# Optimization experiments

Measured on AMD Instinct MI355X. Metric: run time of the kernel, lower is better.

The kernel has to match this reference:

```python
import jax, jax.numpy as jnp
import numpy as np

H, S, D = 64, 64, 4096  # num_heads, head_size, hidden_size (D = H*S)
EPS = 1e-5


def setup_inputs() -> dict:
    key = jax.random.key(0)
    ks = jax.random.split(key, 20)
    n = lambda i, shape, s=1.0: s * jax.random.normal(ks[i], shape, dtype=jnp.float32)
    u = lambda i, shape: jax.random.uniform(ks[i], shape, dtype=jnp.float32)
    return {
        "x": n(0, (D,)),
        "state1": n(1, (D,)),
        "state2": n(2, (H, S, S), 0.1),
        "time_mix_k": u(3, (D,)),
        "time_mix_v": u(4, (D,)),
        "time_mix_r": u(5, (D,)),
        "time_mix_g": u(6, (D,)),
        # time_decay = exp(-exp(raw)) in (0,1); time_first = exp(raw) (time_faaaa-style, kept small)
        "time_decay": jnp.exp(-jnp.exp(n(7, (H, S, 1), 0.5))),
        "time_first": 0.3 * u(8, (H, S, 1)),
        "Wr": n(9, (D, D), 0.02),
        "Wk": n(10, (D, D), 0.01),   # key.weight / 2 baked in
        "Wv": n(11, (D, D), 0.005),  # value.weight / 4 baked in
        "Wg": n(12, (D, D), 0.02),
        "Wo": n(13, (D, D), 0.02),
        "ln1_w": 1.0 + n(14, (D,), 0.1),
        "ln1_b": n(15, (D,), 0.1),
        "lnx_w": 1.0 + n(16, (D,), 0.1),
        "lnx_b": n(17, (D,), 0.1),
    }


def reference(x, state1, state2, time_mix_k, time_mix_v, time_mix_r, time_mix_g,
              time_decay, time_first, Wr, Wk, Wv, Wg, Wo,
              ln1_w, ln1_b, lnx_w, lnx_b):
    last_x = x
    # ln_1 (nn.LayerNorm affine is identity-init; explicit w/b applied after)
    m = jnp.mean(x)
    var = jnp.mean((x - m) ** 2)
    xx = (x - m) * jax.lax.rsqrt(var + EPS) * ln1_w + ln1_b
    state1_out = xx

    mix = lambda t: state1 * (1.0 - t) + xx * t
    r = (Wr @ mix(time_mix_r)).reshape(H, 1, S)
    k = (Wk @ mix(time_mix_k)).reshape(H, S, 1)
    v = (Wv @ mix(time_mix_v)).reshape(H, 1, S)
    g_lin = Wg @ mix(time_mix_g)
    gate = g_lin * jax.nn.sigmoid(g_lin)  # SiLU

    kv = jnp.matmul(k, v)                              # [H, S, S] outer products
    wkv = jnp.matmul(r, kv * time_first + state2)       # [H, 1, S]
    state2_out = kv + state2 * time_decay

    # InstanceNorm2d over (1, S) spatial dims per head, no affine, biased var
    mu = jnp.mean(wkv, axis=(1, 2), keepdims=True)
    vv = jnp.mean((wkv - mu) ** 2, axis=(1, 2), keepdims=True)
    xn = ((wkv - mu) * jax.lax.rsqrt(vv + EPS)).reshape(D)
    y = (xn * lnx_w + lnx_b) * gate
    out = last_x + Wo @ y
    return (out, state1_out, state2_out)
```

## Files before the change

### kernel.cpp

```cpp
#include <hip/hip_runtime.h>
#include <math.h>

#define D 4096
#define H 64
#define S 64
#define EPS 1e-5f

__device__ __forceinline__ float wave_reduce_sum(float v) {
#pragma unroll
    for (int off = 32; off > 0; off >>= 1) v += __shfl_down(v, off, 64);
    return v;
}

__global__ __launch_bounds__(1024) void k_ln_mix(
    const float* __restrict__ x, const float* __restrict__ state1,
    const float* __restrict__ tmk, const float* __restrict__ tmv,
    const float* __restrict__ tmr, const float* __restrict__ tmg,
    const float* __restrict__ ln1w, const float* __restrict__ ln1b,
    float* __restrict__ state1_out, float* __restrict__ mix ) {
    __shared__ float red[32];
    __shared__ float mb[2];
    const int tid = threadIdx.x;
    float xv[4];
    float s = 0.f, sq = 0.f;
#pragma unroll
    for (int k = 0; k < 4; ++k) {
        float v = x[k * 1024 + tid];
        xv[k] = v;
        s += v;
        sq += v * v;
    }
    s = wave_reduce_sum(s);
    sq = wave_reduce_sum(sq);
    const int wave = tid >> 6, lane = tid & 63;
    if (lane == 0) { red[wave] = s; red[16 + wave] = sq; }
    __syncthreads();
    if (tid == 0) {
        float ts = 0.f, tq = 0.f;
        for (int i = 0; i < 16; ++i) { ts += red[i]; tq += red[16 + i]; }
        float m = ts / (float)D;
        float var = tq / (float)D - m * m;
        mb[0] = m;
        mb[1] = rsqrtf(var + EPS);
    }
    __syncthreads();
    const float m = mb[0], rs = mb[1];
#pragma unroll
    for (int k = 0; k < 4; ++k) {
        int i = k * 1024 + tid;
        float xx = (xv[k] - m) * rs * ln1w[i] + ln1b[i];
        state1_out[i] = xx;
        float s1 = state1[i];
        float d = xx - s1;
        mix[i]         = s1 + d * tmr[i];
        mix[D + i]     = s1 + d * tmk[i];
        mix[2 * D + i] = s1 + d * tmv[i];
        mix[3 * D + i] = s1 + d * tmg[i];
    }
}

__global__ __launch_bounds__(256) void k_gemv4(
    const float* __restrict__ Wr, const float* __restrict__ Wk,
    const float* __restrict__ Wv, const float* __restrict__ Wg,
    const float* __restrict__ mix, float* __restrict__ rkvg) {
    const int wave = threadIdx.x >> 6, lane = threadIdx.x & 63;
    const int g = blockIdx.x * 4 + wave;
    const int m = g >> 12;
    const int row = g & (D - 1);
    const float* W = (m == 0) ? Wr : (m == 1) ? Wk : (m == 2) ? Wv : Wg;
    const float4* wr = (const float4*)(W + (size_t)row * D);
    const float4* vx = (const float4*)(mix + (size_t)m * D);
    float a0 = 0.f, a1 = 0.f, a2 = 0.f, a3 = 0.f;
#pragma unroll
    for (int it = 0; it < 16; ++it) {
        float4 w = wr[it * 64 + lane];
        float4 xv = vx[it * 64 + lane];
        a0 += w.x * xv.x; a1 += w.y * xv.y; a2 += w.z * xv.z; a3 += w.w * xv.w;
    }
    float acc = (a0 + a1) + (a2 + a3);
    acc = wave_reduce_sum(acc);
    if (lane == 0) rkvg[m * D + row] = acc;
}

__global__ __launch_bounds__(256) void k_heads(
    const float* __restrict__ rkvg, const float* __restrict__ state2,
    const float* __restrict__ tdecay, const float* __restrict__ tfirst,
    const float* __restrict__ lnxw, const float* __restrict__ lnxb,
    float* __restrict__ state2_out, float* __restrict__ y) {
    __shared__ float part[4][64];
    const int h = blockIdx.x;
    const int wave = threadIdx.x >> 6, j = threadIdx.x & 63;
    const int base = h * S;
    const float rj = rkvg[base + j];
    const float kj = rkvg[D + base + j];
    const float vj = rkvg[2 * D + base + j];
    const float tfj = tfirst[base + j];
    const float tdj = tdecay[base + j];
    const float* s2 = state2 + (size_t)h * S * S;
    float* s2o = state2_out + (size_t)h * S * S;
    float wkv = 0.f;
#pragma unroll
    for (int ii = 0; ii < 16; ++ii) {
        int i = wave * 16 + ii;
        float ri = __shfl(rj, i, 64);
        float ki = __shfl(kj, i, 64);
        float tfi = __shfl(tfj, i, 64);
        float tdi = __shfl(tdj, i, 64);
        float sv = s2[i * S + j];
        float kv = ki * vj;
        wkv += ri * (kv * tfi + sv);
        s2o[i * S + j] = kv + sv * tdi;
    }
    part[wave][j] = wkv;
    __syncthreads();
    if (wave == 0) {
        float w0 = part[0][j] + part[1][j] + part[2][j] + part[3][j];
        float sum = w0, sq = w0 * w0;
#pragma unroll
        for (int off = 1; off < 64; off <<= 1) {
            sum += __shfl_xor(sum, off, 64);
            sq += __shfl_xor(sq, off, 64);
        }
        float mu = sum / (float)S;
        float var = sq / (float)S - mu * mu;
        float xn = (w0 - mu) * rsqrtf(var + EPS);
        float gj = rkvg[3 * D + base + j];
        float gate = gj / (1.f + expf(-gj));
        y[base + j] = (xn * lnxw[base + j] + lnxb[base + j]) * gate;
    }
}

__global__ __launch_bounds__(256) void k_out(
    const float* __restrict__ Wo, const float* __restrict__ y,
    const float* __restrict__ x, float* __restrict__ out) {
    const int wave = threadIdx.x >> 6, lane = threadIdx.x & 63;
    const int row = blockIdx.x * 4 + wave;
    const float4* wr = (const float4*)(Wo + (size_t)row * D);
    const float4* vy = (const float4*)y;
    float a0 = 0.f, a1 = 0.f, a2 = 0.f, a3 = 0.f;
#pragma unroll
    for (int it = 0; it < 16; ++it) {
        float4 w = wr[it * 64 + lane];
        float4 yv = vy[it * 64 + lane];
        a0 += w.x * yv.x; a1 += w.y * yv.y; a2 += w.z * yv.z; a3 += w.w * yv.w;
    }
    float acc = (a0 + a1) + (a2 + a3);
    acc = wave_reduce_sum(acc);
    if (lane == 0) out[row] = x[row] + acc;
}

extern "C" void kernel_launch(void* const* d_in, const int* in_sizes, int n_in,
                              void* d_out, int out_size, void* d_ws, size_t ws_size,
                              hipStream_t stream) {
    const float* x      = (const float*)d_in[0];
    const float* state1 = (const float*)d_in[1];
    const float* state2 = (const float*)d_in[2];
    const float* tmk    = (const float*)d_in[3];
    const float* tmv    = (const float*)d_in[4];
    const float* tmr    = (const float*)d_in[5];
    const float* tmg    = (const float*)d_in[6];
    const float* tdecay = (const float*)d_in[7];
    const float* tfirst = (const float*)d_in[8];
    const float* Wr     = (const float*)d_in[9];
    const float* Wk     = (const float*)d_in[10];
    const float* Wv     = (const float*)d_in[11];
    const float* Wg     = (const float*)d_in[12];
    const float* Wo     = (const float*)d_in[13];
    const float* ln1w   = (const float*)d_in[14];
    const float* ln1b   = (const float*)d_in[15];
    const float* lnxw   = (const float*)d_in[16];
    const float* lnxb   = (const float*)d_in[17];

    float* out        = (float*)d_out;
    float* state1_out = out + D;
    float* state2_out = out + 2 * D;

    float* mix  = (float*)d_ws;
    float* rkvg = mix + 4 * D;
    float* y    = rkvg + 4 * D;

    k_ln_mix<<<1, 1024, 0, stream>>>(x, state1, tmk, tmv, tmr, tmg, ln1w, ln1b,
                                     state1_out, mix);
    k_gemv4<<<4096, 256, 0, stream>>>(Wr, Wk, Wv, Wg, mix, rkvg);
    k_heads<<<64, 256, 0, stream>>>(rkvg, state2, tdecay, tfirst, lnxw, lnxb,
                                    state2_out, y);
    k_out<<<1024, 256, 0, stream>>>(Wo, y, x, out);
}
```

Measured before the change: 324.7 us.

## Vectorize LN/mix, two rows per wave GEMVs with LDS vector, widen heads kernel

The LN/mix kernel now uses float4 loads and stores. Both GEMV kernels stage the input vector in shared memory and have each wave compute two rows, with eight float4 weight loads batched per row to increase memory-level parallelism and halve the grid size. The heads kernel uses 1024 threads per head so each wave handles four rows, with the state loads prefetched. The aim is better bandwidth use on the 320 MB weight stream, at the cost of higher register pressure and an extra shared-memory staging barrier.

Result: no change. 322.8 us (-0.6%).

```diff
diff --git a/kernel.cpp b/kernel.cpp
--- a/kernel.cpp
+++ b/kernel.cpp
@@ -21,15 +21,9 @@
     __shared__ float red[32];
     __shared__ float mb[2];
     const int tid = threadIdx.x;
-    float xv[4];
-    float s = 0.f, sq = 0.f;
-#pragma unroll
-    for (int k = 0; k < 4; ++k) {
-        float v = x[k * 1024 + tid];
-        xv[k] = v;
-        s += v;
-        sq += v * v;
-    }
+    const float4 xv = ((const float4*)x)[tid];
+    float s = (xv.x + xv.y) + (xv.z + xv.w);
+    float sq = (xv.x * xv.x + xv.y * xv.y) + (xv.z * xv.z + xv.w * xv.w);
     s = wave_reduce_sum(s);
     sq = wave_reduce_sum(sq);
     const int wave = tid >> 6, lane = tid & 63;
@@ -45,49 +39,79 @@
     }
     __syncthreads();
     const float m = mb[0], rs = mb[1];
-#pragma unroll
-    for (int k = 0; k < 4; ++k) {
-        int i = k * 1024 + tid;
-        float xx = (xv[k] - m) * rs * ln1w[i] + ln1b[i];
-        state1_out[i] = xx;
-        float s1 = state1[i];
-        float d = xx - s1;
-        mix[i]         = s1 + d * tmr[i];
-        mix[D + i]     = s1 + d * tmk[i];
-        mix[2 * D + i] = s1 + d * tmv[i];
-        mix[3 * D + i] = s1 + d * tmg[i];
-    }
+    const float4 w4 = ((const float4*)ln1w)[tid];
+    const float4 b4 = ((const float4*)ln1b)[tid];
+    float4 xx;
+    xx.x = (xv.x - m) * rs * w4.x + b4.x;
+    xx.y = (xv.y - m) * rs * w4.y + b4.y;
+    xx.z = (xv.z - m) * rs * w4.z + b4.z;
+    xx.w = (xv.w - m) * rs * w4.w + b4.w;
+    ((float4*)state1_out)[tid] = xx;
+    const float4 s1 = ((const float4*)state1)[tid];
+    float4 d;
+    d.x = xx.x - s1.x; d.y = xx.y - s1.y; d.z = xx.z - s1.z; d.w = xx.w - s1.w;
+    const float4 tr = ((const float4*)tmr)[tid];
+    const float4 tk = ((const float4*)tmk)[tid];
+    const float4 tv = ((const float4*)tmv)[tid];
+    const float4 tg = ((const float4*)tmg)[tid];
+    float4 o;
+    o.x = s1.x + d.x * tr.x; o.y = s1.y + d.y * tr.y; o.z = s1.z + d.z * tr.z; o.w = s1.w + d.w * tr.w;
+    ((float4*)mix)[tid] = o;
+    o.x = s1.x + d.x * tk.x; o.y = s1.y + d.y * tk.y; o.z = s1.z + d.z * tk.z; o.w = s1.w + d.w * tk.w;
+    ((float4*)mix)[1024 + tid] = o;
+    o.x = s1.x + d.x * tv.x; o.y = s1.y + d.y * tv.y; o.z = s1.z + d.z * tv.z; o.w = s1.w + d.w * tv.w;
+    ((float4*)mix)[2048 + tid] = o;
+    o.x = s1.x + d.x * tg.x; o.y = s1.y + d.y * tg.y; o.z = s1.z + d.z * tg.z; o.w = s1.w + d.w * tg.w;
+    ((float4*)mix)[3072 + tid] = o;
 }
 
 __global__ __launch_bounds__(256) void k_gemv4(
     const float* __restrict__ Wr, const float* __restrict__ Wk,
     const float* __restrict__ Wv, const float* __restrict__ Wg,
     const float* __restrict__ mix, float* __restrict__ rkvg) {
+    __shared__ float4 smix[1024];
     const int wave = threadIdx.x >> 6, lane = threadIdx.x & 63;
-    const int g = blockIdx.x * 4 + wave;
-    const int m = g >> 12;
-    const int row = g & (D - 1);
+    const int wg = blockIdx.x * 4 + wave;
+    const int m = wg >> 11;
+    const int r0 = (wg & 2047) * 2;
     const float* W = (m == 0) ? Wr : (m == 1) ? Wk : (m == 2) ? Wv : Wg;
-    const float4* wr = (const float4*)(W + (size_t)row * D);
-    const float4* vx = (const float4*)(mix + (size_t)m * D);
-    float a0 = 0.f, a1 = 0.f, a2 = 0.f, a3 = 0.f;
-#pragma unroll
-    for (int it = 0; it < 16; ++it) {
-        float4 w = wr[it * 64 + lane];
-        float4 xv = vx[it * 64 + lane];
-        a0 += w.x * xv.x; a1 += w.y * xv.y; a2 += w.z * xv.z; a3 += w.w * xv.w;
-    }
-    float acc = (a0 + a1) + (a2 + a3);
-    acc = wave_reduce_sum(acc);
-    if (lane == 0) rkvg[m * D + row] = acc;
-}
-
-__global__ __launch_bounds__(256) void k_heads(
+    const float4* vx = (const float4*)mix + (m << 10);
+#pragma unroll
+    for (int t = 0; t < 4; ++t) smix[t * 256 + threadIdx.x] = vx[t * 256 + threadIdx.x];
+    __syncthreads();
+    const float4* w0p = (const float4*)W + (size_t)r0 * 1024;
+    const float4* w1p = w0p + 1024;
+    float a0 = 0.f, a1 = 0.f, b0 = 0.f, b1 = 0.f;
+#pragma unroll
+    for (int half = 0; half < 2; ++half) {
+        float4 wa[8], wb[8];
+#pragma unroll
+        for (int u = 0; u < 8; ++u) wa[u] = w0p[(half * 8 + u) * 64 + lane];
+#pragma unroll
+        for (int u = 0; u < 8; ++u) wb[u] = w1p[(half * 8 + u) * 64 + lane];
+#pragma unroll
+        for (int u = 0; u < 8; ++u) {
+            float4 xv = smix[(half * 8 + u) * 64 + lane];
+            a0 += wa[u].x * xv.x + wa[u].y * xv.y;
+            a1 += wa[u].z * xv.z + wa[u].w * xv.w;
+            b0 += wb[u].x * xv.x + wb[u].y * xv.y;
+            b1 += wb[u].z * xv.z + wb[u].w * xv.w;
+        }
+    }
+    float a = wave_reduce_sum(a0 + a1);
+    float b = wave_reduce_sum(b0 + b1);
+    if (lane == 0) {
+        rkvg[m * D + r0] = a;
+        rkvg[m * D + r0 + 1] = b;
+    }
+}
+
+__global__ __launch_bounds__(1024) void k_heads(
     const float* __restrict__ rkvg, const float* __restrict__ state2,
     const float* __restrict__ tdecay, const float* __restrict__ tfirst,
     const float* __restrict__ lnxw, const float* __restrict__ lnxb,
     float* __restrict__ state2_out, float* __restrict__ y) {
-    __shared__ float part[4][64];
+    __shared__ float part[16][64];
     const int h = blockIdx.x;
     const int wave = threadIdx.x >> 6, j = threadIdx.x & 63;
     const int base = h * S;
@@ -98,23 +122,27 @@
     const float tdj = tdecay[base + j];
     const float* s2 = state2 + (size_t)h * S * S;
     float* s2o = state2_out + (size_t)h * S * S;
+    float sv[4];
+#pragma unroll
+    for (int ii = 0; ii < 4; ++ii) sv[ii] = s2[(wave * 4 + ii) * S + j];
     float wkv = 0.f;
 #pragma unroll
-    for (int ii = 0; ii < 16; ++ii) {
-        int i = wave * 16 + ii;
+    for (int ii = 0; ii < 4; ++ii) {
+        const int i = wave * 4 + ii;
         float ri = __shfl(rj, i, 64);
         float ki = __shfl(kj, i, 64);
         float tfi = __shfl(tfj, i, 64);
         float tdi = __shfl(tdj, i, 64);
-        float sv = s2[i * S + j];
         float kv = ki * vj;
-        wkv += ri * (kv * tfi + sv);
-        s2o[i * S + j] = kv + sv * tdi;
+        wkv += ri * (kv * tfi + sv[ii]);
+        s2o[i * S + j] = kv + sv[ii] * tdi;
     }
     part[wave][j] = wkv;
     __syncthreads();
     if (wave == 0) {
-        float w0 = part[0][j] + part[1][j] + part[2][j] + part[3][j];
+        float w0 = 0.f;
+#pragma unroll
+        for (int t = 0; t < 16; ++t) w0 += part[t][j];
         float sum = w0, sq = w0 * w0;
 #pragma unroll
         for (int off = 1; off < 64; off <<= 1) {
@@ -133,20 +161,39 @@
 __global__ __launch_bounds__(256) void k_out(
     const float* __restrict__ Wo, const float* __restrict__ y,
     const float* __restrict__ x, float* __restrict__ out) {
+    __shared__ float4 sy[1024];
     const int wave = threadIdx.x >> 6, lane = threadIdx.x & 63;
-    const int row = blockIdx.x * 4 + wave;
-    const float4* wr = (const float4*)(Wo + (size_t)row * D);
+    const int wg = blockIdx.x * 4 + wave;
+    const int r0 = wg * 2;
     const float4* vy = (const float4*)y;
-    float a0 = 0.f, a1 = 0.f, a2 = 0.f, a3 = 0.f;
-#pragma unroll
-    for (int it = 0; it < 16; ++it) {
-        float4 w = wr[it * 64 + lane];
-        float4 yv = vy[it * 64 + lane];
-        a0 += w.x * yv.x; a1 += w.y * yv.y; a2 += w.z * yv.z; a3 += w.w * yv.w;
-    }
-    float acc = (a0 + a1) + (a2 + a3);
-    acc = wave_reduce_sum(acc);
-    if (lane == 0) out[row] = x[row] + acc;
+#pragma unroll
+    for (int t = 0; t < 4; ++t) sy[t * 256 + threadIdx.x] = vy[t * 256 + threadIdx.x];
+    __syncthreads();
+    const float4* w0p = (const float4*)Wo + (size_t)r0 * 1024;
+    const float4* w1p = w0p + 1024;
+    float a0 = 0.f, a1 = 0.f, b0 = 0.f, b1 = 0.f;
+#pragma unroll
+    for (int half = 0; half < 2; ++half) {
+        float4 wa[8], wb[8];
+#pragma unroll
+        for (int u = 0; u < 8; ++u) wa[u] = w0p[(half * 8 + u) * 64 + lane];
+#pragma unroll
+        for (int u = 0; u < 8; ++u) wb[u] = w1p[(half * 8 + u) * 64 + lane];
+#pragma unroll
+        for (int u = 0; u < 8; ++u) {
+            float4 xv = sy[(half * 8 + u) * 64 + lane];
+            a0 += wa[u].x * xv.x + wa[u].y * xv.y;
+            a1 += wa[u].z * xv.z + wa[u].w * xv.w;
+            b0 += wb[u].x * xv.x + wb[u].y * xv.y;
+            b1 += wb[u].z * xv.z + wb[u].w * xv.w;
+        }
+    }
+    float a = wave_reduce_sum(a0 + a1);
+    float b = wave_reduce_sum(b0 + b1);
+    if (lane == 0) {
+        out[r0] = x[r0] + a;
+        out[r0 + 1] = x[r0 + 1] + b;
+    }
 }
 
 extern "C" void kernel_launch(void* const* d_in, const int* in_sizes, int n_in,
@@ -181,8 +228,8 @@
 
     k_ln_mix<<<1, 1024, 0, stream>>>(x, state1, tmk, tmv, tmr, tmg, ln1w, ln1b,
                                      state1_out, mix);
-    k_gemv4<<<4096, 256, 0, stream>>>(Wr, Wk, Wv, Wg, mix, rkvg);
-    k_heads<<<64, 256, 0, stream>>>(rkvg, state2, tdecay, tfirst, lnxw, lnxb,
-                                    state2_out, y);
-    k_out<<<1024, 256, 0, stream>>>(Wo, y, x, out);
-}
+    k_gemv4<<<2048, 256, 0, stream>>>(Wr, Wk, Wv, Wg, mix, rkvg);
+    k_heads<<<64, 1024, 0, stream>>>(rkvg, state2, tdecay, tfirst, lnxw, lnxb,
+                                     state2_out, y);
+    k_out<<<512, 256, 0, stream>>>(Wo, y, x, out);
+}
```
